# Performance work log

Measured on AMD Instinct MI355X. Metric: run time of the kernel, lower is better.

## Reference

```python
import jax, jax.numpy as jnp
import numpy as np

B, CIN, COUT, G, HEADS = 4, 256, 256, 8, 4
K, S, P = 7, 1, 3
H = W = 32
IN_W = CIN // G
OUT_W = COUT // G


def setup_inputs() -> dict:
    key = jax.random.key(0)
    ks = jax.random.split(key, 9)
    def n(k, shape, scale=1.0):
        return jax.random.normal(k, shape, dtype=jnp.float32) * scale
    # kaiming fan_out init for the 1x1 convs (fan_out = out channels)
    return {
        "x": n(ks[0], (B, CIN, H, W)),
        "wq": n(ks[1], (G, OUT_W * HEADS, IN_W), (2.0 / (OUT_W * HEADS)) ** 0.5),
        "bq": n(ks[2], (G, OUT_W * HEADS), 0.01),
        "wk": n(ks[3], (G, OUT_W, IN_W), (2.0 / OUT_W) ** 0.5),
        "bk": n(ks[4], (G, OUT_W), 0.01),
        "wv": n(ks[5], (G, OUT_W, IN_W), (2.0 / OUT_W) ** 0.5),
        "bv": n(ks[6], (G, OUT_W), 0.01),
        "rel_h": n(ks[7], (OUT_W // 2, 1, 1, G, K, 1)),
        "rel_w": n(ks[8], (OUT_W // 2, 1, 1, G, 1, K)),
    }


def _sparse_conv(x, w, b):
    # grouped 1x1 conv, groups stacked on last axis (matches torch.stack(dim=-1))
    # x: [B, G*I, h, w]; w: [G, O, I]; b: [G, O] -> [B, O, h, w, G]
    Bn, C, hh, ww = x.shape
    xr = x.reshape(Bn, G, C // G, hh, ww)
    out = jnp.einsum('bgihw,goi->bohwg', xr, w)
    return out + b.T[None, :, None, None, :]


def _unfold(x5, k, s):
    # x5: [B, C, Hp, Wp, G] -> [B, C, Ho, Wo, G, k, k]  (torch unfold(2).unfold(3))
    Bn, C, Hp, Wp, Gn = x5.shape
    Ho = (Hp - k) // s + 1
    Wo = (Wp - k) // s + 1
    patches = jnp.stack(
        [x5[:, :, i:i + (Ho - 1) * s + 1:s, j:j + (Wo - 1) * s + 1:s, :]
         for i in range(k) for j in range(k)], axis=-1)
    return patches.reshape(Bn, C, Ho, Wo, Gn, k, k)


def reference(x, wq, bq, wk, bk, wv, bv, rel_h, rel_w):
    xp = jnp.pad(x, ((0, 0), (0, 0), (P, P), (P, P)))
    q = _sparse_conv(x, wq, bq)    # [B, OUT_W*HEADS, H, W, G]
    k = _sparse_conv(xp, wk, bk)   # [B, OUT_W, Hp, Wp, G] (bias at padded locations, as in torch)
    v = _sparse_conv(xp, wv, bv)
    k = _unfold(k, K, S)           # [B, OUT_W, H, W, G, K, K]
    v = _unfold(v, K, S)
    kh, kw = jnp.split(k, 2, axis=1)
    k = jnp.concatenate([kh + rel_h, kw + rel_w], axis=1)
    kf = k.reshape(B, OUT_W, H, W, G * K * K)
    vf = v.reshape(B, OUT_W, H, W, G * K * K)
    q = q.reshape(B, HEADS, OUT_W, H, W, G)
    # scores: sum over channel c; softmax over flattened (group, kh, kw) window
    scores = jnp.einsum('bhcxyg,bcxym->bhxygm', q, kf)
    attn = jax.nn.softmax(scores, axis=-1)
    # weighted sum over window m and heads h (matches sum(dim=1) then sum(dim=-1))
    out = jnp.einsum('bhxygm,bcxym->bcxyg', attn, vf)   # [B, OUT_W, H, W, G]
    out = jnp.transpose(out, (0, 4, 2, 3, 1)).reshape(B, -1, H, W)  # transpose(1,-1)+reshape
    return out
```

## Files before the change

### kernel.cpp

```cpp
#include <hip/hip_runtime.h>
#include <math.h>

typedef _Float16 f16;
typedef _Float16 f16x4 __attribute__((ext_vector_type(4)));
typedef _Float16 f16x8 __attribute__((ext_vector_type(8)));
typedef __bf16 bf16x2 __attribute__((ext_vector_type(2)));
typedef __bf16 bf16x4a4 __attribute__((ext_vector_type(4), aligned(4)));
typedef __bf16 bf16x8 __attribute__((ext_vector_type(8)));
typedef __bf16 bf16x8a4 __attribute__((ext_vector_type(8), aligned(4)));
typedef float f32x4 __attribute__((ext_vector_type(4)));

#define MFMA_F16(a, b, c)  __builtin_amdgcn_mfma_f32_16x16x32_f16(a, b, c, 0, 0, 0)
#define MFMA_BF16(a, b, c) __builtin_amdgcn_mfma_f32_16x16x32_bf16(a, b, c, 0, 0, 0)

static __device__ inline f16x8 cvt8(const float* p) {
    const float4* p4 = (const float4*)p;
    float4 u0 = p4[0], u1 = p4[1];
    f16x8 r;
    r[0] = (f16)u0.x; r[1] = (f16)u0.y; r[2] = (f16)u0.z; r[3] = (f16)u0.w;
    r[4] = (f16)u1.x; r[5] = (f16)u1.y; r[6] = (f16)u1.z; r[7] = (f16)u1.w;
    return r;
}

__global__ __launch_bounds__(256) void produce_kernel(
    const float* __restrict__ x,
    const float* __restrict__ wq, const float* __restrict__ bq,
    const float* __restrict__ wk, const float* __restrict__ bk,
    const float* __restrict__ wv, const float* __restrict__ bv,
    const float* __restrict__ rel_h, const float* __restrict__ rel_w,
    f16* __restrict__ Qb, f16* __restrict__ Kb,
    __bf16* __restrict__ VtA, __bf16* __restrict__ VtB,
    f16* __restrict__ relp) {
    int bid = blockIdx.x;
    int t = threadIdx.x;

    if (bid == 1216) {
        for (int idx = t; idx < 448 * 32; idx += 256) {
            int c = idx & 31, key = idx >> 5;
            int kw = key & 7, ghk = key >> 3;
            int gp = (ghk * 37) >> 8;
            int kh = ghk - gp * 7;
            float v = 0.f;
            if (kw < 7)
                v = (c < 16) ? rel_h[c * 56 + gp * 7 + kh]
                             : rel_w[(c - 16) * 56 + gp * 7 + kw];
            relp[idx] = (f16)v;
        }
        return;
    }

    int hp = bid % 38, g = (bid / 38) & 7, b = bid / 304;
    bool hin = (hp >= 3 && hp < 35);
    size_t kvbase = (size_t)(b * 8 + g);

    if (!hin) {
        for (int idx = t; idx < 38 * 32; idx += 256) {
            int wp = idx >> 5, c = idx & 31;
            Kb[((kvbase * 38 + hp) * 38 + wp) * 32 + c] = (f16)bk[g * 32 + c];
        }
        for (int idx = t; idx < 40 * 32; idx += 256) {
            int i = idx >> 5, c = idx & 31;
            size_t vo = ((kvbase * 32 + c) * 38 + hp) * 40;
            __bf16 bb = (__bf16)bv[g * 32 + c];
            VtA[vo + i] = (i < 38) ? bb : (__bf16)0.f;
            VtB[vo + i] = (i < 37) ? bb : (__bf16)0.f;
        }
        return;
    }

    int h = hp - 3;
    __shared__ __align__(16) f16 xTl[32 * 40];

    {
        int ic = t >> 3, w = (t & 7) * 4;
        float4 xv = *(const float4*)(x + (((size_t)b * 256 + g * 32 + ic) * 32 + h) * 32 + w);
        xTl[(w + 0) * 40 + ic] = (f16)xv.x;
        xTl[(w + 1) * 40 + ic] = (f16)xv.y;
        xTl[(w + 2) * 40 + ic] = (f16)xv.z;
        xTl[(w + 3) * 40 + ic] = (f16)xv.w;
    }
    __syncthreads();

    int l15 = t & 15, quad = (t >> 4) & 3, wave = t >> 6;

    f16x8 xf0 = *(const f16x8*)(xTl + l15 * 40 + quad * 8);
    f16x8 xf1 = *(const f16x8*)(xTl + (16 + l15) * 40 + quad * 8);

#pragma unroll
    for (int i = 0; i < 2; ++i) {
        int mq = wave * 2 + i;
        f16x8 wf = cvt8(wq + ((size_t)g * 128 + mq * 16 + l15) * 32 + quad * 8);
        float4 b4 = *(const float4*)(bq + g * 128 + mq * 16 + quad * 4);
#pragma unroll
        for (int Nt = 0; Nt < 2; ++Nt) {
            f32x4 d = {0.f, 0.f, 0.f, 0.f};
            d = MFMA_F16(wf, Nt ? xf1 : xf0, d);
            f16x4 q4;
            q4[0] = (f16)(d[0] + b4.x); q4[1] = (f16)(d[1] + b4.y);
            q4[2] = (f16)(d[2] + b4.z); q4[3] = (f16)(d[3] + b4.w);
            int w = Nt * 16 + l15;
            *(f16x4*)(Qb + (size_t)((b * 32 + h) * 32 + w) * 1024 + g * 128 + mq * 16 + quad * 4) = q4;
        }
    }

    if (wave < 2) {
        f16x8 wf = cvt8(wk + ((size_t)g * 32 + wave * 16 + l15) * 32 + quad * 8);
        float4 b4 = *(const float4*)(bk + g * 32 + wave * 16 + quad * 4);
#pragma unroll
        for (int Nt = 0; Nt < 2; ++Nt) {
            f32x4 d = {0.f, 0.f, 0.f, 0.f};
            d = MFMA_F16(wf, Nt ? xf1 : xf0, d);
            f16x4 k4;
            k4[0] = (f16)(d[0] + b4.x); k4[1] = (f16)(d[1] + b4.y);
            k4[2] = (f16)(d[2] + b4.z); k4[3] = (f16)(d[3] + b4.w);
            int wp = Nt * 16 + l15 + 3;
            *(f16x4*)(Kb + ((kvbase * 38 + hp) * 38 + wp) * 32 + wave * 16 + quad * 4) = k4;
        }
    } else {
        int Nt = wave - 2;
        f16x8 wf = cvt8(wv + ((size_t)g * 32 + Nt * 16 + l15) * 32 + quad * 8);
        float bias = bv[g * 32 + Nt * 16 + l15];
        int c = Nt * 16 + l15;
        size_t vo = ((kvbase * 32 + c) * 38 + hp) * 40;
#pragma unroll
        for (int Mt = 0; Mt < 2; ++Mt) {
            f32x4 d = {0.f, 0.f, 0.f, 0.f};
            d = MFMA_F16(Mt ? xf1 : xf0, wf, d);
            __bf16 v0 = (__bf16)(d[0] + bias), v1 = (__bf16)(d[1] + bias);
            __bf16 v2 = (__bf16)(d[2] + bias), v3 = (__bf16)(d[3] + bias);
            int wp0 = Mt * 16 + quad * 4 + 3;
            VtA[vo + wp0] = v0;
            bf16x2 mid; mid[0] = v1; mid[1] = v2;
            *(bf16x2*)(VtA + vo + wp0 + 1) = mid;
            VtA[vo + wp0 + 3] = v3;
            bf16x4a4 p4; p4[0] = v0; p4[1] = v1; p4[2] = v2; p4[3] = v3;
            *(bf16x4a4*)(VtB + vo + wp0 - 1) = p4;
        }
    }

    for (int idx = t; idx < 192; idx += 256) {
        int wi = idx >> 5, c = idx & 31;
        int wp = (wi < 3) ? wi : (32 + wi);
        Kb[((kvbase * 38 + hp) * 38 + wp) * 32 + c] = (f16)bk[g * 32 + c];
        size_t vo = ((kvbase * 32 + c) * 38 + hp) * 40;
        __bf16 bb = (__bf16)bv[g * 32 + c];
        VtA[vo + wp] = bb;
        if (wp >= 1) VtB[vo + wp - 1] = bb;
    }
    for (int idx = t; idx < 160; idx += 256) {
        int c = idx / 5, j = idx % 5;
        size_t vo = ((kvbase * 32 + c) * 38 + hp) * 40;
        if (j < 2) VtA[vo + 38 + j] = (__bf16)0.f;
        else       VtB[vo + 35 + j] = (__bf16)0.f;
    }
}

__global__ __launch_bounds__(64, 4) void attn_kernel(
    const f16* __restrict__ Qb, const f16* __restrict__ Kb,
    const __bf16* __restrict__ VtA, const __bf16* __restrict__ VtB,
    const f16* __restrict__ relp, float* __restrict__ out) {
    int bid = blockIdx.x;
    int pid = (bid & 7) * 512 + (bid >> 3);
    int y = pid & 31, x = (pid >> 5) & 31, b = pid >> 10;

    __shared__ __align__(16) __bf16 Pl[32 * 136];

    int t = threadIdx.x;
    int l15 = t & 15, quad = t >> 4, kwl = t & 7;
    bool mask7 = (kwl == 7);

    {
        int row = t >> 1, off = 112 + (t & 1) * 8;
        *(uint4*)(Pl + row * 136 + off) = (uint4){0u, 0u, 0u, 0u};
    }

    f16x8 qf[2];
    {
        const f16* qp = Qb + (size_t)pid * 1024;
        qf[0] = *(const f16x8*)(qp + l15 * 32 + quad * 8);
        qf[1] = *(const f16x8*)(qp + (16 + l15) * 32 + quad * 8);
    }

    float fsum[2][4];
#pragma unroll
    for (int m = 0; m < 2; ++m)
#pragma unroll
        for (int r = 0; r < 4; ++r) fsum[m][r] = 0.f;

    f32x4 acc[2][2];
#pragma unroll
    for (int m = 0; m < 2; ++m)
#pragma unroll
        for (int n = 0; n < 2; ++n) acc[m][n] = (f32x4){0.f, 0.f, 0.f, 0.f};

    int yk = y + kwl;
    if (yk > 37) yk = 37;
    const __bf16* __restrict__ Vsel = (y & 1) ? VtB : VtA;
    int yv = y & ~1;

    for (int chunk = 0; chunk < 4; ++chunk) {
        int gp = chunk * 2 + ((t >> 3) & 1);
        const f16* kbp = Kb + ((((size_t)(b * 8 + gp) * 38 + x) * 38 + yk) << 5) + quad * 8;
        const f16* rpp = relp + (size_t)(gp * 7 * 8 + kwl) * 32 + quad * 8;
#pragma unroll
        for (int kh = 0; kh < 7; ++kh) {
            f16x8 kb = *(const f16x8*)kbp;
            f16x8 rp = *(const f16x8*)rpp;
            kbp += 38 * 32;
            rpp += 256;
            kb += rp;
#pragma unroll
            for (int Mt = 0; Mt < 2; ++Mt) {
                f32x4 d = {0.f, 0.f, 0.f, 0.f};
                d = MFMA_F16(qf[Mt], kb, d);
#pragma unroll
                for (int r = 0; r < 4; ++r) {
                    float e = __expf(d[r]);
                    e = mask7 ? 0.f : e;
                    fsum[Mt][r] += e;
                    Pl[(Mt * 16 + quad * 4 + r) * 136 + kh * 16 + l15] = (__bf16)e;
                }
            }
        }

        int gpv = chunk * 2 + (quad & 1);
        int qh = quad >> 1;
#pragma unroll
        for (int ks = 0; ks < 4; ++ks) {
            bf16x8 af0 = *(const bf16x8*)(Pl + l15 * 136 + ks * 32 + quad * 8);
            bf16x8 af1 = *(const bf16x8*)(Pl + (16 + l15) * 136 + ks * 32 + quad * 8);
            int kh = 2 * ks + qh;
            int khc = (kh > 6) ? 6 : kh;
#pragma unroll
            for (int t2 = 0; t2 < 2; ++t2) {
                const __bf16* vp =
                    Vsel + (((size_t)(b * 8 + gpv) * 32 + t2 * 16 + l15) * 38 + x + khc) * 40 + yv;
                bf16x8a4 bv8 = *(const bf16x8a4*)vp;
                bv8[7] = (__bf16)0.0f;
                acc[0][t2] = MFMA_BF16(af0, (bf16x8)bv8, acc[0][t2]);
                acc[1][t2] = MFMA_BF16(af1, (bf16x8)bv8, acc[1][t2]);
            }
        }
    }

#pragma unroll
    for (int dlt = 1; dlt < 16; dlt <<= 1)
#pragma unroll
        for (int m = 0; m < 2; ++m)
#pragma unroll
            for (int r = 0; r < 4; ++r) fsum[m][r] += __shfl_xor(fsum[m][r], dlt);

    float inv[2][4];
#pragma unroll
    for (int m = 0; m < 2; ++m)
#pragma unroll
        for (int r = 0; r < 4; ++r) inv[m][r] = 1.0f / fsum[m][r];

#pragma unroll
    for (int Mt = 0; Mt < 2; ++Mt)
#pragma unroll
        for (int t2 = 0; t2 < 2; ++t2) {
            float o = 0.f;
#pragma unroll
            for (int r = 0; r < 4; ++r) o = fmaf(acc[Mt][t2][r], inv[Mt][r], o);
            int g = Mt * 4 + quad;
            out[(((size_t)(b * 8 + g) * 32 + x) * 32 + y) * 32 + t2 * 16 + l15] = o;
        }
}

extern "C" void kernel_launch(void* const* d_in, const int* in_sizes, int n_in,
                              void* d_out, int out_size, void* d_ws, size_t ws_size,
                              hipStream_t stream) {
    const float* x     = (const float*)d_in[0];
    const float* wq    = (const float*)d_in[1];
    const float* bq    = (const float*)d_in[2];
    const float* wk    = (const float*)d_in[3];
    const float* bk    = (const float*)d_in[4];
    const float* wv    = (const float*)d_in[5];
    const float* bv    = (const float*)d_in[6];
    const float* rel_h = (const float*)d_in[7];
    const float* rel_w = (const float*)d_in[8];
    float* out = (float*)d_out;

    unsigned char* ws = (unsigned char*)d_ws;
    f16*    Qb   = (f16*)ws;
    f16*    Kb   = (f16*)(ws + 8388608);
    __bf16* VtA  = (__bf16*)(ws + 8388608 + 2957312);
    __bf16* VtB  = (__bf16*)(ws + 8388608 + 2957312 + 3112960);
    f16*    relp = (f16*)(ws + 8388608 + 2957312 + 3112960 + 3112960);

    hipLaunchKernelGGL(produce_kernel, dim3(1217), dim3(256), 0, stream,
                       x, wq, bq, wk, bk, wv, bv, rel_h, rel_w, Qb, Kb, VtA, VtB, relp);
    hipLaunchKernelGGL(attn_kernel, dim3(4096), dim3(64), 0, stream,
                       Qb, Kb, VtA, VtB, relp, out);
}
```

Measured before the change: 125.0 us.

## Keep softmax probabilities in registers by transposing score MFMA and chaining into PV

```diff
diff --git a/kernel.cpp b/kernel.cpp
--- a/kernel.cpp
+++ b/kernel.cpp
@@ -5,13 +5,14 @@
 typedef _Float16 f16x4 __attribute__((ext_vector_type(4)));
 typedef _Float16 f16x8 __attribute__((ext_vector_type(8)));
 typedef __bf16 bf16x2 __attribute__((ext_vector_type(2)));
+typedef __bf16 bf16x4 __attribute__((ext_vector_type(4)));
 typedef __bf16 bf16x4a4 __attribute__((ext_vector_type(4), aligned(4)));
-typedef __bf16 bf16x8 __attribute__((ext_vector_type(8)));
-typedef __bf16 bf16x8a4 __attribute__((ext_vector_type(8), aligned(4)));
+typedef short s16x4 __attribute__((ext_vector_type(4)));
+typedef short s16x4a4 __attribute__((ext_vector_type(4), aligned(4)));
 typedef float f32x4 __attribute__((ext_vector_type(4)));
 
 #define MFMA_F16(a, b, c)  __builtin_amdgcn_mfma_f32_16x16x32_f16(a, b, c, 0, 0, 0)
-#define MFMA_BF16(a, b, c) __builtin_amdgcn_mfma_f32_16x16x32_bf16(a, b, c, 0, 0, 0)
+#define MFMA_BF16_K16(a, b, c) __builtin_amdgcn_mfma_f32_16x16x16bf16_1k(a, b, c, 0, 0, 0)
 
 static __device__ inline f16x8 cvt8(const float* p) {
     const float4* p4 = (const float4*)p;
@@ -155,24 +156,21 @@
     }
 }
 
-__global__ __launch_bounds__(64, 4) void attn_kernel(
+__global__ __launch_bounds__(128, 4) void attn_kernel(
     const f16* __restrict__ Qb, const f16* __restrict__ Kb,
     const __bf16* __restrict__ VtA, const __bf16* __restrict__ VtB,
     const f16* __restrict__ relp, float* __restrict__ out) {
     int bid = blockIdx.x;
-    int pid = (bid & 7) * 512 + (bid >> 3);
+    int t = threadIdx.x;
+    int wvi = t >> 6;
+    int pid = ((bid & 7) * 256 + (bid >> 3)) * 2 + wvi;
     int y = pid & 31, x = (pid >> 5) & 31, b = pid >> 10;
 
-    __shared__ __align__(16) __bf16 Pl[32 * 136];
-
-    int t = threadIdx.x;
-    int l15 = t & 15, quad = t >> 4, kwl = t & 7;
-    bool mask7 = (kwl == 7);
-
-    {
-        int row = t >> 1, off = 112 + (t & 1) * 8;
-        *(uint4*)(Pl + row * 136 + off) = (uint4){0u, 0u, 0u, 0u};
-    }
+    int lane = t & 63;
+    int l15 = lane & 15, quad = lane >> 4, kwl = lane & 7, p8 = (lane >> 3) & 1;
+    bool oddq = (quad & 1);
+    int kw0 = (quad & 1) * 4;
+    int gph = quad >> 1;
 
     f16x8 qf[2];
     {
@@ -181,90 +179,75 @@
         qf[1] = *(const f16x8*)(qp + (16 + l15) * 32 + quad * 8);
     }
 
-    float fsum[2][4];
-#pragma unroll
-    for (int m = 0; m < 2; ++m)
-#pragma unroll
-        for (int r = 0; r < 4; ++r) fsum[m][r] = 0.f;
-
+    float fsumT[2] = {0.f, 0.f};
     f32x4 acc[2][2];
 #pragma unroll
-    for (int m = 0; m < 2; ++m)
-#pragma unroll
-        for (int n = 0; n < 2; ++n) acc[m][n] = (f32x4){0.f, 0.f, 0.f, 0.f};
+    for (int ct = 0; ct < 2; ++ct)
+#pragma unroll
+        for (int m = 0; m < 2; ++m) acc[ct][m] = (f32x4){0.f, 0.f, 0.f, 0.f};
 
     int yk = y + kwl;
     if (yk > 37) yk = 37;
     const __bf16* __restrict__ Vsel = (y & 1) ? VtB : VtA;
-    int yv = y & ~1;
+    int yv = (y & ~1) + kw0;
 
     for (int chunk = 0; chunk < 4; ++chunk) {
-        int gp = chunk * 2 + ((t >> 3) & 1);
-        const f16* kbp = Kb + ((((size_t)(b * 8 + gp) * 38 + x) * 38 + yk) << 5) + quad * 8;
-        const f16* rpp = relp + (size_t)(gp * 7 * 8 + kwl) * 32 + quad * 8;
+        int gpr = chunk * 2 + p8;
+        int gpv = chunk * 2 + gph;
+        const f16* kbp = Kb + ((((size_t)(b * 8 + gpr) * 38 + x) * 38 + yk) << 5) + quad * 8;
+        const f16* rpp = relp + ((size_t)(gpr * 56 + kwl) << 5) + quad * 8;
+        const __bf16* vp0 = Vsel + (((size_t)(b * 8 + gpv) * 32 + l15) * 38 + x) * 40 + yv;
+        const __bf16* vp1 = vp0 + (size_t)16 * 38 * 40;
 #pragma unroll
         for (int kh = 0; kh < 7; ++kh) {
-            f16x8 kb = *(const f16x8*)kbp;
-            f16x8 rp = *(const f16x8*)rpp;
-            kbp += 38 * 32;
-            rpp += 256;
+            f16x8 kb = *(const f16x8*)kbp;  kbp += 38 * 32;
+            f16x8 rp = *(const f16x8*)rpp;  rpp += 256;
             kb += rp;
+            s16x4a4 vf0 = *(const s16x4a4*)vp0;  vp0 += 40;
+            s16x4a4 vf1 = *(const s16x4a4*)vp1;  vp1 += 40;
 #pragma unroll
             for (int Mt = 0; Mt < 2; ++Mt) {
                 f32x4 d = {0.f, 0.f, 0.f, 0.f};
-                d = MFMA_F16(qf[Mt], kb, d);
-#pragma unroll
-                for (int r = 0; r < 4; ++r) {
-                    float e = __expf(d[r]);
-                    e = mask7 ? 0.f : e;
-                    fsum[Mt][r] += e;
-                    Pl[(Mt * 16 + quad * 4 + r) * 136 + kh * 16 + l15] = (__bf16)e;
-                }
+                d = MFMA_F16(kb, qf[Mt], d);
+                float e0 = __expf(d[0]);
+                float e1 = __expf(d[1]);
+                float e2 = __expf(d[2]);
+                float e3 = oddq ? 0.f : __expf(d[3]);
+                fsumT[Mt] += (e0 + e1) + (e2 + e3);
+                bf16x4 pb;
+                pb[0] = (__bf16)e0; pb[1] = (__bf16)e1;
+                pb[2] = (__bf16)e2; pb[3] = (__bf16)e3;
+                s16x4 pbi = __builtin_bit_cast(s16x4, pb);
+                acc[0][Mt] = MFMA_BF16_K16((s16x4)vf0, pbi, acc[0][Mt]);
+                acc[1][Mt] = MFMA_BF16_K16((s16x4)vf1, pbi, acc[1][Mt]);
             }
         }
-
-        int gpv = chunk * 2 + (quad & 1);
-        int qh = quad >> 1;
-#pragma unroll
-        for (int ks = 0; ks < 4; ++ks) {
-            bf16x8 af0 = *(const bf16x8*)(Pl + l15 * 136 + ks * 32 + quad * 8);
-            bf16x8 af1 = *(const bf16x8*)(Pl + (16 + l15) * 136 + ks * 32 + quad * 8);
-            int kh = 2 * ks + qh;
-            int khc = (kh > 6) ? 6 : kh;
-#pragma unroll
-            for (int t2 = 0; t2 < 2; ++t2) {
-                const __bf16* vp =
-                    Vsel + (((size_t)(b * 8 + gpv) * 32 + t2 * 16 + l15) * 38 + x + khc) * 40 + yv;
-                bf16x8a4 bv8 = *(const bf16x8a4*)vp;
-                bv8[7] = (__bf16)0.0f;
-                acc[0][t2] = MFMA_BF16(af0, (bf16x8)bv8, acc[0][t2]);
-                acc[1][t2] = MFMA_BF16(af1, (bf16x8)bv8, acc[1][t2]);
+    }
+
+#pragma unroll
+    for (int m = 0; m < 2; ++m) {
+        fsumT[m] += __shfl_xor(fsumT[m], 16);
+        fsumT[m] += __shfl_xor(fsumT[m], 32);
+    }
+    float inv[2] = {1.0f / fsumT[0], 1.0f / fsumT[1]};
+
+#pragma unroll
+    for (int Mt = 0; Mt < 2; ++Mt)
+#pragma unroll
+        for (int ct = 0; ct < 2; ++ct) {
+            float v[4];
+#pragma unroll
+            for (int r = 0; r < 4; ++r) {
+                v[r] = acc[ct][Mt][r] * inv[Mt];
+                v[r] += __shfl_xor(v[r], 1);
+                v[r] += __shfl_xor(v[r], 2);
             }
-        }
-    }
-
-#pragma unroll
-    for (int dlt = 1; dlt < 16; dlt <<= 1)
-#pragma unroll
-        for (int m = 0; m < 2; ++m)
-#pragma unroll
-            for (int r = 0; r < 4; ++r) fsum[m][r] += __shfl_xor(fsum[m][r], dlt);
-
-    float inv[2][4];
-#pragma unroll
-    for (int m = 0; m < 2; ++m)
-#pragma unroll
-        for (int r = 0; r < 4; ++r) inv[m][r] = 1.0f / fsum[m][r];
-
-#pragma unroll
-    for (int Mt = 0; Mt < 2; ++Mt)
-#pragma unroll
-        for (int t2 = 0; t2 < 2; ++t2) {
-            float o = 0.f;
-#pragma unroll
-            for (int r = 0; r < 4; ++r) o = fmaf(acc[Mt][t2][r], inv[Mt][r], o);
-            int g = Mt * 4 + quad;
-            out[(((size_t)(b * 8 + g) * 32 + x) * 32 + y) * 32 + t2 * 16 + l15] = o;
+            if ((l15 & 3) == 0) {
+                int g = Mt * 4 + (l15 >> 2);
+                float4 o4 = {v[0], v[1], v[2], v[3]};
+                *(float4*)(out + ((((size_t)(b * 8 + g) * 32 + x) * 32 + y) << 5) +
+                           ct * 16 + quad * 4) = o4;
+            }
         }
 }
 
@@ -291,6 +274,6 @@
 
     hipLaunchKernelGGL(produce_kernel, dim3(1217), dim3(256), 0, stream,
                        x, wq, bq, wk, bk, wv, bv, rel_h, rel_w, Qb, Kb, VtA, VtB, relp);
-    hipLaunchKernelGGL(attn_kernel, dim3(4096), dim3(64), 0, stream,
+    hipLaunchKernelGGL(attn_kernel, dim3(2048), dim3(128), 0, stream,
                        Qb, Kb, VtA, VtB, relp, out);
 }
```

Measured after the change: 130.0 us. 4.0% more time.
